# Kernel optimization log

Hardware: AMD Instinct MI355X
Metric: run time of the kernel (lower is better)

## Reference

```python
import jax, jax.numpy as jnp
import numpy as np

N, DIN, D, K, H, N_ITERS = 16384, 256, 1024, 64, 2048, 3
THRESH = 0.3
EPS = 1e-8


def layernorm(x):
    mu = jnp.mean(x, axis=-1, keepdims=True)
    var = jnp.var(x, axis=-1, keepdims=True)
    return (x - mu) * jax.lax.rsqrt(var + 1e-5)


def setup_inputs() -> dict:
    key = jax.random.key(0)
    ks = jax.random.split(key, 20)
    s = 0.02
    return {
        "detections_t": jax.random.normal(ks[0], (N, DIN), jnp.float32),
        "detections_t1": jax.random.normal(ks[1], (N, DIN), jnp.float32),
        "W_enc": s * jax.random.normal(ks[2], (DIN, D), jnp.float32),
        "b_enc": jnp.zeros((D,), jnp.float32),
        "Wq": s * jax.random.normal(ks[3], (D, D), jnp.float32),
        "bq": jnp.zeros((D,), jnp.float32),
        "Wk": s * jax.random.normal(ks[4], (D, D), jnp.float32),
        "bk": jnp.zeros((D,), jnp.float32),
        "Wv": s * jax.random.normal(ks[5], (D, D), jnp.float32),
        "bv": jnp.zeros((D,), jnp.float32),
        "Wi": s * jax.random.normal(ks[6], (3 * D, D), jnp.float32),  # GRU input weights
        "Wh": s * jax.random.normal(ks[7], (3 * D, D), jnp.float32),  # GRU hidden weights
        "bi": jnp.zeros((3 * D,), jnp.float32),
        "bh": jnp.zeros((3 * D,), jnp.float32),
        "W1": s * jax.random.normal(ks[8], (D, H), jnp.float32),
        "b1": jnp.zeros((H,), jnp.float32),
        "W2": s * jax.random.normal(ks[9], (H, D), jnp.float32),
        "b2": jnp.zeros((D,), jnp.float32),
        "slots_mu": s * jax.random.normal(ks[10], (1, D), jnp.float32),
        "init_noise": jax.random.normal(ks[11], (K, D), jnp.float32) * s,
    }


def _gru(u, h, Wi, Wh, bi, bh):
    gi = u @ Wi.T + bi          # [K, 3D]
    gh = h @ Wh.T + bh
    ir, iz, inn = jnp.split(gi, 3, axis=-1)
    hr, hz, hn = jnp.split(gh, 3, axis=-1)
    r = jax.nn.sigmoid(ir + hr)
    z = jax.nn.sigmoid(iz + hz)
    n = jnp.tanh(inn + r * hn)
    return (1.0 - z) * n + z * h


def _process_frame(dets, prev_slots, p):
    x = layernorm(dets @ p["W_enc"] + p["b_enc"])          # [N, D]
    k = x @ p["Wk"] + p["bk"]                               # [N, D]
    v = x @ p["Wv"] + p["bv"]                               # [N, D]
    slots = prev_slots if prev_slots is not None else p["slots_mu"] + p["init_noise"]
    scale = D ** -0.5
    for _ in range(N_ITERS):
        slots_prev = slots
        q = layernorm(slots) @ p["Wq"] + p["bq"]            # [K, D]
        dots = (q @ k.T) * scale                             # [K, N]
        attn = jax.nn.softmax(dots, axis=0)                  # slots compete per detection
        attn = attn / (jnp.sum(attn, axis=-1, keepdims=True) + EPS)
        updates = attn @ v                                   # [K, D]
        slots = _gru(updates, slots_prev, p["Wi"], p["Wh"], p["bi"], p["bh"])
        slots = slots + (jax.nn.relu(layernorm(slots) @ p["W1"] + p["b1"]) @ p["W2"] + p["b2"])
    return slots


def _slot_similarity(a, b):
    an = a / (jnp.linalg.norm(a, axis=-1, keepdims=True) + EPS)
    bn = b / (jnp.linalg.norm(b, axis=-1, keepdims=True) + EPS)
    return an @ bn.T                                         # [K, K]


def _greedy_match(sim):
    max_sims = jnp.max(sim, axis=1)
    max_idxs = jnp.argmax(sim, axis=1)
    order = jnp.argsort(-max_sims)
    def step(carry, idx):
        matches, used = carry
        j = max_idxs[idx]
        ok = jnp.logical_and(~used[j], max_sims[idx] > THRESH)
        matches = matches.at[idx].set(jnp.where(ok, j, matches[idx]))
        used = used.at[j].set(used[j] | ok)
        return (matches, used), None
    init = (jnp.full((K,), -1, jnp.int32), jnp.zeros((K,), jnp.bool_))
    (matches, _), _ = jax.lax.scan(step, init, order)
    return matches


def reference(detections_t, detections_t1, W_enc, b_enc, Wq, bq, Wk, bk, Wv, bv,
              Wi, Wh, bi, bh, W1, b1, W2, b2, slots_mu, init_noise):
    p = dict(W_enc=W_enc, b_enc=b_enc, Wq=Wq, bq=bq, Wk=Wk, bk=bk, Wv=Wv, bv=bv,
             Wi=Wi, Wh=Wh, bi=bi, bh=bh, W1=W1, b1=b1, W2=W2, b2=b2,
             slots_mu=slots_mu, init_noise=init_noise)
    prev_slots = _process_frame(detections_t, None, p)
    curr_slots = _process_frame(detections_t1, prev_slots, p)
    sim = _slot_similarity(prev_slots, curr_slots)
    matches = _greedy_match(sim)
    return matches, sim
```

## Files before the change

kernel.cpp:

```cpp
#include <hip/hip_runtime.h>
#include <hip/hip_bf16.h>
#include <type_traits>

typedef __hip_bfloat16 bf16;
typedef __attribute__((ext_vector_type(8))) short s16x8;
typedef __attribute__((ext_vector_type(4))) float f32x4;

#define N_DET 16384
#define DIN   256
#define DD    1024
#define KSLOT 64
#define HH    2048
#define TD    3072

__device__ __forceinline__ float b2f(bf16 x){ return __bfloat162float(x); }
__device__ __forceinline__ bf16  f2b(float x){ return __float2bfloat16(x); }
__device__ __forceinline__ float bits2f(short u){ return __uint_as_float(((unsigned)(unsigned short)u) << 16); }

__device__ __forceinline__ void gload_lds16(const void* g, void* l) {
  __builtin_amdgcn_global_load_lds(
      (const __attribute__((address_space(1))) unsigned int*)g,
      (__attribute__((address_space(3))) unsigned int*)l, 16, 0, 0);
}

__device__ __forceinline__ void big_compute(bf16* As, bf16* Bs,
    const bf16* __restrict__ Ap, const bf16* __restrict__ Bp, int K, f32x4 acc[4][4])
{
  const int tid = threadIdx.x;
  const int lane = tid & 63, wave = tid >> 6;
  const int wr = wave >> 1, wc = wave & 1;
  const int l15 = lane & 15, h = lane >> 4;
  const int rr = tid >> 3;
  const int qs = ((tid & 7) ^ (rr & 7)) * 8;

#pragma unroll
  for (int m = 0; m < 4; ++m)
#pragma unroll
    for (int n = 0; n < 4; ++n) acc[m][n] = {0.f, 0.f, 0.f, 0.f};

  for (int k0 = 0; k0 < K; k0 += 64) {
    __syncthreads();
#pragma unroll
    for (int g = 0; g < 4; ++g)
      gload_lds16(Ap + (size_t)(g * 32 + rr) * K + k0 + qs,
                  As + ((size_t)g * 256 + wave * 64) * 8);
#pragma unroll
    for (int g = 0; g < 4; ++g)
      gload_lds16(Bp + (size_t)(g * 32 + rr) * K + k0 + qs,
                  Bs + ((size_t)g * 256 + wave * 64) * 8);
    __syncthreads();

#pragma unroll
    for (int ks = 0; ks < 2; ++ks) {
      s16x8 af[4], bfr[4];
#pragma unroll
      for (int m = 0; m < 4; ++m) {
        int row = wr * 64 + m * 16 + l15;
        af[m] = *(const s16x8*)&As[row * 64 + (((ks * 4 + h) ^ (l15 & 7)) * 8)];
      }
#pragma unroll
      for (int n = 0; n < 4; ++n) {
        int row = wc * 64 + n * 16 + l15;
        bfr[n] = *(const s16x8*)&Bs[row * 64 + (((ks * 4 + h) ^ (l15 & 7)) * 8)];
      }
#pragma unroll
      for (int m = 0; m < 4; ++m)
#pragma unroll
        for (int n = 0; n < 4; ++n)
          acc[m][n] = __builtin_amdgcn_mfma_f32_16x16x32_bf16(af[m], bfr[n], acc[m][n], 0, 0, 0);
    }
  }
}

__global__ __launch_bounds__(256) void gemm_mfma_bt(
    const bf16* __restrict__ A, const bf16* __restrict__ Bt,
    const float* __restrict__ bias, bf16* __restrict__ C, int M, int N, int K)
{
  const int nct = N >> 7;
  const int chunk = gridDim.x >> 3;
  const int wg = (blockIdx.x & 7) * chunk + (blockIdx.x >> 3);
  const int bn = (wg % nct) * 128;
  const int bm = (wg / nct) * 128;

  __shared__ bf16 As[128 * 64];
  __shared__ bf16 Bs[128 * 64];
  f32x4 acc[4][4];
  big_compute(As, Bs, A + (size_t)bm * K, Bt + (size_t)bn * K, K, acc);

  const int lane = threadIdx.x & 63, wave = threadIdx.x >> 6;
  const int wr = wave >> 1, wc = wave & 1;
#pragma unroll
  for (int m = 0; m < 4; ++m)
#pragma unroll
    for (int n = 0; n < 4; ++n) {
      int col = bn + wc * 64 + n * 16 + (lane & 15);
      float bv = bias ? bias[col] : 0.f;
#pragma unroll
      for (int j = 0; j < 4; ++j) {
        int row = bm + wr * 64 + m * 16 + (lane >> 4) * 4 + j;
        C[(size_t)row * N + col] = f2b(acc[m][n][j] + bv);
      }
    }
}

__device__ __forceinline__ void skinny_compute(bf16* As, bf16* Bs,
    const bf16* __restrict__ A, const bf16* __restrict__ Bt,
    int K, int Kc, int n0, int kb0, f32x4 acc[4])
{
  const int tid = threadIdx.x;
  const int lane = tid & 63, wave = tid >> 6;
  const int rem = wave * 64 + lane;
  const int r = rem >> 2, q = rem & 3;
  const int l15 = lane & 15, h = lane >> 4;

#pragma unroll
  for (int m = 0; m < 4; ++m) acc[m] = {0.f, 0.f, 0.f, 0.f};

  for (int kb = kb0; kb < kb0 + Kc; kb += 128) {
    __syncthreads();
#pragma unroll
    for (int g = 0; g < 4; ++g)
      gload_lds16(A + (size_t)r * K + kb + g * 32 + q * 8,
                  As + ((size_t)g * 256 + wave * 64) * 8);
#pragma unroll
    for (int g = 0; g < 4; ++g)
      gload_lds16(Bt + (size_t)(n0 + r) * K + kb + g * 32 + q * 8,
                  Bs + ((size_t)g * 256 + wave * 64) * 8);
    __syncthreads();

#pragma unroll
    for (int ks = 0; ks < 4; ++ks) {
      s16x8 bfr = *(const s16x8*)&Bs[(ks * 64 + wave * 16 + l15) * 32 + h * 8];
#pragma unroll
      for (int m = 0; m < 4; ++m) {
        s16x8 af = *(const s16x8*)&As[(ks * 64 + m * 16 + l15) * 32 + h * 8];
        acc[m] = __builtin_amdgcn_mfma_f32_16x16x32_bf16(af, bfr, acc[m], 0, 0, 0);
      }
    }
  }
}

template<int EPI>
__global__ __launch_bounds__(256) void gemm_skinny_e(
    const bf16* __restrict__ A, const bf16* __restrict__ Bt,
    float* __restrict__ pbuf, bf16* __restrict__ outb,
    const float* __restrict__ bias, int N, int K, int Kc)
{
  __shared__ bf16 As[4 * 64 * 32];
  __shared__ bf16 Bs[4 * 64 * 32];
  f32x4 acc[4];
  skinny_compute(As, Bs, A, Bt, K, Kc, blockIdx.x * 64, blockIdx.y * Kc, acc);

  const int lane = threadIdx.x & 63, wave = threadIdx.x >> 6;
  const int l15 = lane & 15, h = lane >> 4;
#pragma unroll
  for (int m = 0; m < 4; ++m)
#pragma unroll
    for (int j = 0; j < 4; ++j) {
      int row = m * 16 + h * 4 + j;
      int col = blockIdx.x * 64 + wave * 16 + l15;
      if (EPI == 0) {
        pbuf[((size_t)(blockIdx.y * 64) + row) * N + col] = acc[m][j];
      } else {
        float v = acc[m][j] + bias[col];
        if (EPI == 2) v = fmaxf(v, 0.f);
        outb[(size_t)row * N + col] = f2b(v);
      }
    }
}

__global__ __launch_bounds__(256) void gemm_skinny_dual(
    const bf16* __restrict__ A0, const bf16* __restrict__ A1,
    const bf16* __restrict__ B0, const bf16* __restrict__ B1,
    float* __restrict__ p0, float* __restrict__ p1, int N, int K, int Kc)
{
  __shared__ bf16 As[4 * 64 * 32];
  __shared__ bf16 Bs[4 * 64 * 32];
  const bf16* A = blockIdx.z ? A1 : A0;
  const bf16* B = blockIdx.z ? B1 : B0;
  float* p = blockIdx.z ? p1 : p0;

  f32x4 acc[4];
  skinny_compute(As, Bs, A, B, K, Kc, blockIdx.x * 64, blockIdx.y * Kc, acc);

  const int lane = threadIdx.x & 63, wave = threadIdx.x >> 6;
  const int l15 = lane & 15, h = lane >> 4;
#pragma unroll
  for (int m = 0; m < 4; ++m)
#pragma unroll
    for (int j = 0; j < 4; ++j) {
      int row = m * 16 + h * 4 + j;
      int col = blockIdx.x * 64 + wave * 16 + l15;
      p[((size_t)(blockIdx.y * 64) + row) * N + col] = acc[m][j];
    }
}

__device__ __forceinline__ void block_ln_store(float v[4], float s, float sq,
    bf16* __restrict__ out, int row,
    const float* __restrict__ wqbk, float* __restrict__ cbuf, float* __restrict__ colsum)
{
  for (int o = 32; o > 0; o >>= 1) { s += __shfl_down(s, o, 64); sq += __shfl_down(sq, o, 64); }
  __shared__ float ls[4], lq[4];
  int w = threadIdx.x >> 6;
  if ((threadIdx.x & 63) == 0) { ls[w] = s; lq[w] = sq; }
  __syncthreads();
  s  = ls[0] + ls[1] + ls[2] + ls[3];
  sq = lq[0] + lq[1] + lq[2] + lq[3];
  float mu = s * (1.f / DD);
  float var = sq * (1.f / DD) - mu * mu;
  float rstd = rsqrtf(var + 1e-5f);
#pragma unroll
  for (int j = 0; j < 4; j++)
    out[(size_t)row * DD + threadIdx.x + j * 256] = f2b((v[j] - mu) * rstd);
  if (wqbk) {
    float dot = 0.f;
#pragma unroll
    for (int j = 0; j < 4; j++) dot += (v[j] - mu) * rstd * wqbk[threadIdx.x + j * 256];
    for (int o = 32; o > 0; o >>= 1) dot += __shfl_down(dot, o, 64);
    __syncthreads();
    if ((threadIdx.x & 63) == 0) ls[w] = dot;
    __syncthreads();
    if (threadIdx.x == 0) { cbuf[row] = ls[0] + ls[1] + ls[2] + ls[3]; colsum[row] = 0.f; }
  }
}

__global__ __launch_bounds__(256) void gru_reduce_ln(const float* __restrict__ pA,
    const float* __restrict__ pB, const float* __restrict__ bvi,
    const float* __restrict__ bh, float* __restrict__ slots, bf16* __restrict__ lnb)
{
  int s = blockIdx.x, t = threadIdx.x;
  float v[4], sum = 0.f, sq = 0.f;
#pragma unroll
  for (int j = 0; j < 4; ++j) {
    int d = t + j * 256;
    const float* a = pA + (size_t)s * TD;
    const float* b = pB + (size_t)s * TD;
    float ir = bvi[d] + a[d], iz = bvi[1024 + d] + a[1024 + d], in_ = bvi[2048 + d] + a[2048 + d];
    float hr = bh[d] + b[d], hz = bh[1024 + d] + b[1024 + d], hnn = bh[2048 + d] + b[2048 + d];
    float r = 1.f / (1.f + expf(-(ir + hr)));
    float z = 1.f / (1.f + expf(-(iz + hz)));
    float nn = tanhf(in_ + r * hnn);
    float h = slots[(size_t)s * DD + d];
    float hv = (1.f - z) * nn + z * h;
    slots[(size_t)s * DD + d] = hv;
    v[j] = hv; sum += hv; sq += hv * hv;
  }
  block_ln_store(v, sum, sq, lnb, s, nullptr, nullptr, nullptr);
}

template<int SK>
__global__ __launch_bounds__(256) void mlp2_reduce_ln(const float* __restrict__ pbuf,
    const float* __restrict__ bias, float* __restrict__ slots,
    bf16* __restrict__ slotspb, bf16* __restrict__ lnb,
    const float* __restrict__ wqbk, float* __restrict__ cbuf, float* __restrict__ colsum)
{
  int s = blockIdx.x, t = threadIdx.x;
  float v[4], sum = 0.f, sq = 0.f;
#pragma unroll
  for (int j = 0; j < 4; ++j) {
    int d = t + j * 256;
    float x = bias[d] + slots[(size_t)s * DD + d];
#pragma unroll
    for (int sk = 0; sk < SK; ++sk) x += pbuf[(size_t)(sk * 64 + s) * DD + d];
    slots[(size_t)s * DD + d] = x;
    slotspb[(size_t)s * DD + d] = f2b(x);
    v[j] = x; sum += x; sq += x * x;
  }
  block_ln_store(v, sum, sq, lnb, s, wqbk, cbuf, colsum);
}

__global__ __launch_bounds__(256) void slots_init_ln(const float* __restrict__ mu,
    const float* __restrict__ noise, float* __restrict__ slots,
    bf16* __restrict__ slotspb, bf16* __restrict__ lnb,
    const float* __restrict__ wqbk, float* __restrict__ cbuf, float* __restrict__ colsum)
{
  int s = blockIdx.x, t = threadIdx.x;
  float v[4], sum = 0.f, sq = 0.f;
#pragma unroll
  for (int j = 0; j < 4; ++j) {
    int d = t + j * 256;
    float x = mu[d] + noise[(size_t)s * DD + d];
    slots[(size_t)s * DD + d] = x;
    slotspb[(size_t)s * DD + d] = f2b(x);
    v[j] = x; sum += x; sq += x * x;
  }
  block_ln_store(v, sum, sq, lnb, s, wqbk, cbuf, colsum);
}

__global__ __launch_bounds__(256) void qk_softmax(const bf16* __restrict__ qkb,
    const bf16* __restrict__ x, const float* __restrict__ cbuf,
    bf16* __restrict__ attn, float* __restrict__ colsum)
{
  __shared__ bf16 Qs[64 * 64];
  __shared__ bf16 Ks[64 * 64];
  __shared__ float cs[64], cl[64];
  const int t = threadIdx.x, lane = t & 63, wave = t >> 6;
  const int n0 = blockIdx.x * 64;
  const int l15 = lane & 15, h = lane >> 4;
  if (t < 64) { cs[t] = 0.f; cl[t] = cbuf[t]; }

  f32x4 acc[4];
#pragma unroll
  for (int m = 0; m < 4; ++m) acc[m] = {0.f, 0.f, 0.f, 0.f};

  for (int k0 = 0; k0 < DD; k0 += 64) {
    __syncthreads();
#pragma unroll
    for (int c = 0; c < 2; ++c) {
      int i = c * 256 + t;
      int r = i >> 3, q8 = i & 7;
      gload_lds16(qkb + (size_t)r * DD + k0 + q8 * 8, Qs + ((size_t)c * 256 + wave * 64) * 8);
    }
#pragma unroll
    for (int c = 0; c < 2; ++c) {
      int i = c * 256 + t;
      int r = i >> 3, q8 = i & 7;
      gload_lds16(x + (size_t)(n0 + r) * DD + k0 + q8 * 8, Ks + ((size_t)c * 256 + wave * 64) * 8);
    }
    __syncthreads();

#pragma unroll
    for (int ks = 0; ks < 2; ++ks) {
      s16x8 bfr = *(const s16x8*)&Ks[(wave * 16 + l15) * 64 + ks * 32 + h * 8];
#pragma unroll
      for (int m = 0; m < 4; ++m) {
        s16x8 af = *(const s16x8*)&Qs[(m * 16 + l15) * 64 + ks * 32 + h * 8];
        acc[m] = __builtin_amdgcn_mfma_f32_16x16x32_bf16(af, bfr, acc[m], 0, 0, 0);
      }
    }
  }

  float e[4][4];
  float cmax = -1e30f;
#pragma unroll
  for (int m = 0; m < 4; ++m)
#pragma unroll
    for (int j = 0; j < 4; ++j) {
      e[m][j] = (acc[m][j] + cl[m * 16 + h * 4 + j]) * 0.03125f;
      cmax = fmaxf(cmax, e[m][j]);
    }
  cmax = fmaxf(cmax, __shfl_xor(cmax, 16, 64));
  cmax = fmaxf(cmax, __shfl_xor(cmax, 32, 64));
  float ssum = 0.f;
#pragma unroll
  for (int m = 0; m < 4; ++m)
#pragma unroll
    for (int j = 0; j < 4; ++j) { e[m][j] = expf(e[m][j] - cmax); ssum += e[m][j]; }
  ssum += __shfl_xor(ssum, 16, 64);
  ssum += __shfl_xor(ssum, 32, 64);
  float inv = 1.f / ssum;
  __syncthreads();

  const int n = n0 + wave * 16 + l15;
#pragma unroll
  for (int m = 0; m < 4; ++m)
#pragma unroll
    for (int j = 0; j < 4; ++j) {
      float a = e[m][j] * inv;
      int s = m * 16 + h * 4 + j;
      attn[(size_t)s * N_DET + n] = f2b(a);
      float v = a;
      v += __shfl_xor(v, 1, 64);
      v += __shfl_xor(v, 2, 64);
      v += __shfl_xor(v, 4, 64);
      v += __shfl_xor(v, 8, 64);
      if (l15 == 0) atomicAdd(&cs[s], v);
    }
  __syncthreads();
  if (t < 64) atomicAdd(&colsum[t], cs[t]);
}

template<int SK>
__global__ __launch_bounds__(256) void updates_reduce2(const float* __restrict__ pbuf,
    const float* __restrict__ colsum, bf16* __restrict__ tb)
{
  int s = blockIdx.y, d = blockIdx.x * 256 + threadIdx.x;
  float v = 0.f;
#pragma unroll
  for (int sk = 0; sk < SK; ++sk) v += pbuf[(size_t)(sk * 64 + s) * DD + d];
  tb[(size_t)s * DD + d] = f2b(v / (colsum[s] + 1e-8f));
}

__global__ __launch_bounds__(256) void transpose_w(const float* __restrict__ W,
                                                   bf16* __restrict__ Wt, int K, int N)
{
  __shared__ float t[32][33];
  int n0 = blockIdx.x * 32, k0 = blockIdx.y * 32;
  int tx = threadIdx.x & 31, ty = threadIdx.x >> 5;
  for (int r = ty; r < 32; r += 8)
    t[r][tx] = W[(size_t)(k0 + r) * N + n0 + tx];
  __syncthreads();
  for (int r = ty; r < 32; r += 8)
    Wt[(size_t)(n0 + r) * K + k0 + tx] = f2b(t[tx][r]);
}

__global__ void f32_to_bf16_v(const float* __restrict__ in, bf16* __restrict__ out, int n)
{
  int i = (blockIdx.x * 256 + threadIdx.x) * 4;
  if (i < n) {
    float4 v = *(const float4*)(in + i);
    bf16 o[4] = {f2b(v.x), f2b(v.y), f2b(v.z), f2b(v.w)};
    *(ushort4*)(out + i) = *(const ushort4*)o;
  }
}

__global__ void convert_all(const float* __restrict__ Wh, const float* __restrict__ Wi,
    const float* __restrict__ Wv, const float* __restrict__ Wq, const float* __restrict__ Wk,
    bf16* __restrict__ oWh, bf16* __restrict__ oWi, bf16* __restrict__ oWv,
    bf16* __restrict__ oWq, bf16* __restrict__ oWk)
{
  int b = blockIdx.x;
  const float* src; bf16* dst; int base;
  if      (b < 3072) { src = Wh; dst = oWh; base = b; }
  else if (b < 6144) { src = Wi; dst = oWi; base = b - 3072; }
  else if (b < 7168) { src = Wv; dst = oWv; base = b - 6144; }
  else if (b < 8192) { src = Wq; dst = oWq; base = b - 7168; }
  else               { src = Wk; dst = oWk; base = b - 8192; }
  int i = (base * 256 + threadIdx.x) * 4;
  float4 v = *(const float4*)(src + i);
  bf16 o[4] = {f2b(v.x), f2b(v.y), f2b(v.z), f2b(v.w)};
  *(ushort4*)(dst + i) = *(const ushort4*)o;
}

__global__ void matvec3(const float* __restrict__ Wi, const float* __restrict__ Wq,
    const float* __restrict__ Wk, const float* __restrict__ bv, const float* __restrict__ bk,
    const float* __restrict__ bq, const float* __restrict__ bi,
    float* __restrict__ bvi, float* __restrict__ wqbk, float* __restrict__ bqk)
{
  int i = blockIdx.x * 256 + threadIdx.x;
  const float* w; const float* vec; float s; float* out; int idx;
  if (i < 3072)      { idx = i;        w = Wi + (size_t)idx * DD; vec = bv; s = bi[idx]; out = bvi; }
  else if (i < 4096) { idx = i - 3072; w = Wq + (size_t)idx * DD; vec = bk; s = 0.f;     out = wqbk; }
  else               { idx = i - 4096; w = Wk + (size_t)idx * DD; vec = bq; s = 0.f;     out = bqk; }
  for (int k = 0; k < DD; k += 4) {
    float4 wv = *(const float4*)(w + k);
    float4 bb = *(const float4*)(vec + k);
    s += wv.x * bb.x + wv.y * bb.y + wv.z * bb.z + wv.w * bb.w;
  }
  out[idx] = s;
}

__global__ __launch_bounds__(256) void transpose_x(const bf16* __restrict__ in, bf16* __restrict__ out)
{
  __shared__ bf16 t[64][72];
  int n0 = blockIdx.x * 64, d0 = blockIdx.y * 64;
  int r = threadIdx.x >> 2, c = (threadIdx.x & 3) * 16;
  s16x8 v0 = *(const s16x8*)&in[(size_t)(n0 + r) * DD + d0 + c];
  s16x8 v1 = *(const s16x8*)&in[(size_t)(n0 + r) * DD + d0 + c + 8];
  const bf16* p0 = (const bf16*)&v0;
  const bf16* p1 = (const bf16*)&v1;
#pragma unroll
  for (int j = 0; j < 8; ++j) { t[c + j][r] = p0[j]; t[c + 8 + j][r] = p1[j]; }
  __syncthreads();
  bf16 o[16];
#pragma unroll
  for (int j = 0; j < 16; ++j) o[j] = t[r][c + j];
  *(s16x8*)&out[(size_t)(d0 + r) * N_DET + n0 + c]     = *(const s16x8*)&o[0];
  *(s16x8*)&out[(size_t)(d0 + r) * N_DET + n0 + c + 8] = *(const s16x8*)&o[8];
}

__global__ __launch_bounds__(256) void ln_rows2(const bf16* __restrict__ in, bf16* __restrict__ out)
{
  int r = blockIdx.x * 2 + (threadIdx.x >> 7);
  int t7 = threadIdx.x & 127;
  s16x8 vv = *(const s16x8*)(in + (size_t)r * DD + t7 * 8);
  float f[8], s = 0.f, sq = 0.f;
#pragma unroll
  for (int j = 0; j < 8; ++j) { f[j] = bits2f(vv[j]); s += f[j]; sq += f[j] * f[j]; }
  for (int o = 32; o > 0; o >>= 1) { s += __shfl_down(s, o, 64); sq += __shfl_down(sq, o, 64); }
  __shared__ float ls[4], lq[4];
  int w = threadIdx.x >> 6;
  if ((threadIdx.x & 63) == 0) { ls[w] = s; lq[w] = sq; }
  __syncthreads();
  int rg = threadIdx.x >> 7;
  s  = ls[rg * 2] + ls[rg * 2 + 1];
  sq = lq[rg * 2] + lq[rg * 2 + 1];
  float mu = s * (1.f / DD);
  float var = sq * (1.f / DD) - mu * mu;
  float rstd = rsqrtf(var + 1e-5f);
  bf16 o[8];
#pragma unroll
  for (int j = 0; j < 8; ++j) o[j] = f2b((f[j] - mu) * rstd);
  *(s16x8*)(out + (size_t)r * DD + t7 * 8) = *(const s16x8*)o;
}

__global__ __launch_bounds__(256) void rownorm2(const float* __restrict__ a,
    const float* __restrict__ b, float* __restrict__ an, float* __restrict__ bn)
{
  int rb = blockIdx.x;
  const float* p = (rb < 64 ? a : b) + (size_t)(rb & 63) * DD;
  float* o = (rb < 64 ? an : bn) + (size_t)(rb & 63) * DD;
  float v[4], sq = 0.f;
#pragma unroll
  for (int j = 0; j < 4; j++) { v[j] = p[threadIdx.x + j*256]; sq += v[j]*v[j]; }
  for (int os = 32; os > 0; os >>= 1) sq += __shfl_down(sq, os, 64);
  __shared__ float lq[4];
  int w = threadIdx.x >> 6;
  if ((threadIdx.x & 63) == 0) lq[w] = sq;
  __syncthreads();
  sq = lq[0] + lq[1] + lq[2] + lq[3];
  float sc = 1.f / (sqrtf(sq) + 1e-8f);
#pragma unroll
  for (int j = 0; j < 4; j++) o[threadIdx.x + j*256] = v[j] * sc;
}

__global__ __launch_bounds__(256) void sim_kernel(const float* __restrict__ an,
    const float* __restrict__ bn, float* __restrict__ simout)
{
  __shared__ float ar[1024];
  int i = blockIdx.x;
  for (int l = threadIdx.x; l < 1024; l += 256) ar[l] = an[(size_t)i * DD + l];
  __syncthreads();
  int j = threadIdx.x >> 2, g = threadIdx.x & 3;
  float sum = 0.f;
  for (int d = g; d < 1024; d += 4) sum += ar[d] * bn[(size_t)j * DD + d];
  sum += __shfl_xor(sum, 1, 64);
  sum += __shfl_xor(sum, 2, 64);
  if (g == 0) simout[i * 64 + j] = sum;
}

__global__ void match_kernel(const float* __restrict__ sim, float* __restrict__ outm)
{
  __shared__ float m[64];
  __shared__ int idx[64];
  __shared__ int order[64];
  __shared__ int used[64];
  int i = threadIdx.x;
  float best = -1e30f; int bj = 0;
  for (int j = 0; j < 64; j++) {
    float v = sim[i * 64 + j];
    if (v > best) { best = v; bj = j; }
  }
  m[i] = best; idx[i] = bj; used[i] = 0;
  __syncthreads();
  int cnt = 0;
  for (int j = 0; j < 64; j++) {
    float mj = m[j];
    if (mj > best || (mj == best && j < i)) cnt++;
  }
  order[cnt] = i;
  __syncthreads();
  if (i == 0) {
    for (int r = 0; r < 64; r++) {
      int ii = order[r];
      int j = idx[ii];
      bool ok = (!used[j]) && (m[ii] > 0.3f);
      outm[ii] = ok ? (float)j : -1.0f;
      if (ok) used[j] = 1;
    }
  }
}

static constexpr size_t OFF_XPRE = 0;
static constexpr size_t OFF_ATT  = 0;
static constexpr size_t OFF_PA   = (size_t)4  << 20;
static constexpr size_t OFF_P0   = (size_t)8  << 20;
static constexpr size_t OFF_P1   = (size_t)10 << 20;
static constexpr size_t OFF_WET  = (size_t)32 << 20;
static constexpr size_t OFF_WQKT = OFF_WET + ((size_t)512 << 10);
static constexpr size_t OFF_W1T  = OFF_WQKT + ((size_t)2 << 20);
static constexpr size_t OFF_W2T  = OFF_W1T + ((size_t)4 << 20);
static constexpr size_t OFF_WHB  = OFF_W2T + ((size_t)4 << 20);
static constexpr size_t OFF_WVIT = OFF_WHB + ((size_t)6 << 20);
static constexpr size_t OFF_X    = (size_t)60 << 20;
static constexpr size_t OFF_WIB  = OFF_X;
static constexpr size_t OFF_WVB  = OFF_X + ((size_t)6 << 20);
static constexpr size_t OFF_WQB  = OFF_X + ((size_t)8 << 20);
static constexpr size_t OFF_WKB  = OFF_X + ((size_t)10 << 20);
static constexpr size_t OFF_DBF  = OFF_X;
static constexpr size_t OFF_XT   = OFF_X + ((size_t)32 << 20);
static constexpr size_t OFF_SM   = OFF_XT + ((size_t)32 << 20);
static constexpr size_t OFF_SL   = OFF_SM;
static constexpr size_t OFF_SLPB = OFF_SL  + 262144;
static constexpr size_t OFF_LNB  = OFF_SLPB + 131072;
static constexpr size_t OFF_QKB  = OFF_LNB + 131072;
static constexpr size_t OFF_TB   = OFF_QKB + 131072;
static constexpr size_t OFF_HIDB = OFF_TB  + 131072;
static constexpr size_t OFF_PRV  = OFF_HIDB + 262144;
static constexpr size_t OFF_AN   = OFF_PRV + 262144;
static constexpr size_t OFF_BN   = OFF_AN  + 262144;
static constexpr size_t OFF_CS   = OFF_BN  + 262144;
static constexpr size_t OFF_BVI  = OFF_CS  + 4096;
static constexpr size_t OFF_WQBK = OFF_BVI + 16384;
static constexpr size_t OFF_BQK  = OFF_WQBK + 4096;

extern "C" void kernel_launch(void* const* d_in, const int* in_sizes, int n_in,
                              void* d_out, int out_size, void* d_ws, size_t ws_size,
                              hipStream_t stream)
{
  (void)in_sizes; (void)n_in; (void)out_size; (void)ws_size;
  const float* dets_t   = (const float*)d_in[0];
  const float* dets_t1  = (const float*)d_in[1];
  const float* W_enc    = (const float*)d_in[2];
  const float* b_enc    = (const float*)d_in[3];
  const float* Wq       = (const float*)d_in[4];
  const float* bq       = (const float*)d_in[5];
  const float* Wk       = (const float*)d_in[6];
  const float* bk       = (const float*)d_in[7];
  const float* Wv       = (const float*)d_in[8];
  const float* bv       = (const float*)d_in[9];
  const float* Wi       = (const float*)d_in[10];
  const float* Wh       = (const float*)d_in[11];
  const float* bi       = (const float*)d_in[12];
  const float* bh       = (const float*)d_in[13];
  const float* W1       = (const float*)d_in[14];
  const float* b1       = (const float*)d_in[15];
  const float* W2       = (const float*)d_in[16];
  const float* b2       = (const float*)d_in[17];
  const float* slots_mu = (const float*)d_in[18];
  const float* init_noise = (const float*)d_in[19];

  char* ws = (char*)d_ws;
  bf16*  x_pre  = (bf16*)(ws + OFF_XPRE);
  bf16*  attn   = (bf16*)(ws + OFF_ATT);
  float* pA     = (float*)(ws + OFF_PA);
  float* p0     = (float*)(ws + OFF_P0);
  float* p1     = (float*)(ws + OFF_P1);
  bf16*  Wenc_t = (bf16*)(ws + OFF_WET);
  bf16*  Wqk_t  = (bf16*)(ws + OFF_WQKT);
  bf16*  W1_t   = (bf16*)(ws + OFF_W1T);
  bf16*  W2_t   = (bf16*)(ws + OFF_W2T);
  bf16*  Wh_b   = (bf16*)(ws + OFF_WHB);
  bf16*  Wvit   = (bf16*)(ws + OFF_WVIT);
  bf16*  Wi_b   = (bf16*)(ws + OFF_WIB);
  bf16*  Wv_bf  = (bf16*)(ws + OFF_WVB);
  bf16*  Wq_bf  = (bf16*)(ws + OFF_WQB);
  bf16*  Wk_bf  = (bf16*)(ws + OFF_WKB);
  bf16*  dets_bf= (bf16*)(ws + OFF_DBF);
  bf16*  x      = (bf16*)(ws + OFF_X);
  bf16*  xT     = (bf16*)(ws + OFF_XT);
  float* slots  = (float*)(ws + OFF_SL);
  bf16*  slotspb= (bf16*)(ws + OFF_SLPB);
  bf16*  lnb    = (bf16*)(ws + OFF_LNB);
  bf16*  qkb    = (bf16*)(ws + OFF_QKB);
  bf16*  tb     = (bf16*)(ws + OFF_TB);
  bf16*  hidb   = (bf16*)(ws + OFF_HIDB);
  float* prevs  = (float*)(ws + OFF_PRV);
  float* an     = (float*)(ws + OFF_AN);
  float* bn     = (float*)(ws + OFF_BN);
  float* colsum = (float*)(ws + OFF_CS);
  float* cbuf   = colsum + 64;
  float* bvi    = (float*)(ws + OFF_BVI);
  float* wqbk   = (float*)(ws + OFF_WQBK);
  float* bqk    = (float*)(ws + OFF_BQK);

  transpose_w<<<dim3(32,  8), 256, 0, stream>>>(W_enc, Wenc_t, DIN, DD);
  transpose_w<<<dim3(64, 32), 256, 0, stream>>>(W1,    W1_t,   DD,  HH);
  transpose_w<<<dim3(32, 64), 256, 0, stream>>>(W2,    W2_t,   HH,  DD);
  convert_all<<<9216, 256, 0, stream>>>(Wh, Wi, Wv, Wq, Wk, Wh_b, Wi_b, Wv_bf, Wq_bf, Wk_bf);
  matvec3<<<20, 256, 0, stream>>>(Wi, Wq, Wk, bv, bk, bq, bi, bvi, wqbk, bqk);
  gemm_mfma_bt<<<192, 256, 0, stream>>>(Wi_b, Wv_bf, nullptr, Wvit, TD, DD, DD);
  gemm_mfma_bt<<<64, 256, 0, stream>>>(Wk_bf, Wq_bf, nullptr, Wqk_t, DD, DD, DD);

  auto frame = [&](const float* dets, bool first) {
    f32_to_bf16_v<<<(N_DET*DIN)/1024, 256, 0, stream>>>(dets, dets_bf, N_DET*DIN);
    gemm_mfma_bt<<<1024, 256, 0, stream>>>(dets_bf, Wenc_t, b_enc, x_pre, N_DET, DD, DIN);
    ln_rows2<<<N_DET/2, 256, 0, stream>>>(x_pre, x);
    transpose_x<<<dim3(256, 16), 256, 0, stream>>>(x, xT);
    if (first) slots_init_ln<<<64, 256, 0, stream>>>(slots_mu, init_noise, slots, slotspb, lnb, wqbk, cbuf, colsum);
    for (int it = 0; it < 3; ++it) {
      gemm_skinny_e<1><<<dim3(16, 1), 256, 0, stream>>>(lnb, Wqk_t, nullptr, qkb, bqk, DD, DD, DD);
      qk_softmax<<<256, 256, 0, stream>>>(qkb, x, cbuf, attn, colsum);
      gemm_skinny_e<0><<<dim3(16, 16), 256, 0, stream>>>(attn, xT, pA, nullptr, nullptr, DD, N_DET, 1024);
      updates_reduce2<16><<<dim3(4, 64), 256, 0, stream>>>(pA, colsum, tb);
      gemm_skinny_dual<<<dim3(48, 1, 2), 256, 0, stream>>>(tb, slotspb, Wvit, Wh_b, p0, p1, TD, DD, DD);
      gru_reduce_ln<<<64, 256, 0, stream>>>(p0, p1, bvi, bh, slots, lnb);
      gemm_skinny_e<2><<<dim3(32, 1), 256, 0, stream>>>(lnb, W1_t, nullptr, hidb, b1, HH, DD, DD);
      gemm_skinny_e<0><<<dim3(16, 2), 256, 0, stream>>>(hidb, W2_t, pA, nullptr, nullptr, DD, HH, 1024);
      mlp2_reduce_ln<2><<<64, 256, 0, stream>>>(pA, b2, slots, slotspb, lnb, wqbk, cbuf, colsum);
    }
  };

  frame(dets_t, true);
  hipMemcpyAsync(prevs, slots, 262144, hipMemcpyDeviceToDevice, stream);
  frame(dets_t1, false);

  rownorm2<<<128, 256, 0, stream>>>(prevs, slots, an, bn);
  float* outf = (float*)d_out;
  sim_kernel<<<KSLOT, 256, 0, stream>>>(an, bn, outf + 64);
  match_kernel<<<1, 64, 0, stream>>>(outf + 64, outf);
}
```

Before: 752.8 us.

## Fuse setup kernels, parallelize matvec per wave, and fuse layernorm with transpose

Merges the three weight transposes into one launch and the two setup GEMMs into one launch. The bias matvec now gives one wavefront per row with coalesced loads, where before each thread walked a whole row serially. Per frame, layernorm and the transpose of x are fused into one kernel that stages 32 rows in LDS and writes both x and xT. This removes a round trip of x through global memory and several launches, but the column reads from the LDS tile in the transpose phase may hit bank conflicts and the large LDS tile limits occupancy.

```diff
diff --git a/kernel.cpp b/kernel.cpp
--- a/kernel.cpp
+++ b/kernel.cpp
@@ -72,18 +72,13 @@
   }
 }
 
-__global__ __launch_bounds__(256) void gemm_mfma_bt(
+__device__ __forceinline__ void big_gemm_body(int wg, int nct,
     const bf16* __restrict__ A, const bf16* __restrict__ Bt,
-    const float* __restrict__ bias, bf16* __restrict__ C, int M, int N, int K)
-{
-  const int nct = N >> 7;
-  const int chunk = gridDim.x >> 3;
-  const int wg = (blockIdx.x & 7) * chunk + (blockIdx.x >> 3);
+    const float* __restrict__ bias, bf16* __restrict__ C, int N, int K,
+    bf16* As, bf16* Bs)
+{
   const int bn = (wg % nct) * 128;
   const int bm = (wg / nct) * 128;
-
-  __shared__ bf16 As[128 * 64];
-  __shared__ bf16 Bs[128 * 64];
   f32x4 acc[4][4];
   big_compute(As, Bs, A + (size_t)bm * K, Bt + (size_t)bn * K, K, acc);
 
@@ -101,6 +96,35 @@
         C[(size_t)row * N + col] = f2b(acc[m][n][j] + bv);
       }
     }
+}
+
+__global__ __launch_bounds__(256) void gemm_mfma_bt(
+    const bf16* __restrict__ A, const bf16* __restrict__ Bt,
+    const float* __restrict__ bias, bf16* __restrict__ C, int M, int N, int K)
+{
+  const int nct = N >> 7;
+  const int chunk = gridDim.x >> 3;
+  const int wg = (blockIdx.x & 7) * chunk + (blockIdx.x >> 3);
+  __shared__ bf16 As[128 * 64];
+  __shared__ bf16 Bs[128 * 64];
+  big_gemm_body(wg, nct, A, Bt, bias, C, N, K, As, Bs);
+}
+
+__global__ __launch_bounds__(256) void gemm_setup_pair(
+    const bf16* __restrict__ Wi_b, const bf16* __restrict__ Wv_bf, bf16* __restrict__ Wvit,
+    const bf16* __restrict__ Wk_bf, const bf16* __restrict__ Wq_bf, bf16* __restrict__ Wqk_t)
+{
+  __shared__ bf16 As[128 * 64];
+  __shared__ bf16 Bs[128 * 64];
+  if (blockIdx.x < 192) {
+    int bid = blockIdx.x;
+    int wg = (bid & 7) * 24 + (bid >> 3);
+    big_gemm_body(wg, 8, Wi_b, Wv_bf, nullptr, Wvit, DD, DD, As, Bs);
+  } else {
+    int bid = blockIdx.x - 192;
+    int wg = (bid & 7) * 8 + (bid >> 3);
+    big_gemm_body(wg, 8, Wk_bf, Wq_bf, nullptr, Wqk_t, DD, DD, As, Bs);
+  }
 }
 
 __device__ __forceinline__ void skinny_compute(bf16* As, bf16* Bs,
@@ -381,11 +405,17 @@
   tb[(size_t)s * DD + d] = f2b(v / (colsum[s] + 1e-8f));
 }
 
-__global__ __launch_bounds__(256) void transpose_w(const float* __restrict__ W,
-                                                   bf16* __restrict__ Wt, int K, int N)
+__global__ __launch_bounds__(256) void transpose_all(const float* __restrict__ W_enc,
+    const float* __restrict__ W1, const float* __restrict__ W2,
+    bf16* __restrict__ Wenc_t, bf16* __restrict__ W1_t, bf16* __restrict__ W2_t)
 {
   __shared__ float t[32][33];
-  int n0 = blockIdx.x * 32, k0 = blockIdx.y * 32;
+  int b = blockIdx.x;
+  const float* W; bf16* Wt; int K, N, bx, by;
+  if (b < 256)       { W = W_enc; Wt = Wenc_t; K = DIN;  N = DD; bx = b & 31;  by = b >> 5; }
+  else if (b < 2304) { int r = b - 256;  W = W1; Wt = W1_t; K = DD;  N = HH; bx = r & 63; by = r >> 6; }
+  else               { int r = b - 2304; W = W2; Wt = W2_t; K = HH;  N = DD; bx = r & 31; by = r >> 5; }
+  int n0 = bx * 32, k0 = by * 32;
   int tx = threadIdx.x & 31, ty = threadIdx.x >> 5;
   for (int r = ty; r < 32; r += 8)
     t[r][tx] = W[(size_t)(k0 + r) * N + n0 + tx];
@@ -422,66 +452,90 @@
   *(ushort4*)(dst + i) = *(const ushort4*)o;
 }
 
-__global__ void matvec3(const float* __restrict__ Wi, const float* __restrict__ Wq,
-    const float* __restrict__ Wk, const float* __restrict__ bv, const float* __restrict__ bk,
-    const float* __restrict__ bq, const float* __restrict__ bi,
+__global__ __launch_bounds__(256) void matvec3_wave(const float* __restrict__ Wi,
+    const float* __restrict__ Wq, const float* __restrict__ Wk,
+    const float* __restrict__ bv, const float* __restrict__ bk, const float* __restrict__ bq,
+    const float* __restrict__ bi,
     float* __restrict__ bvi, float* __restrict__ wqbk, float* __restrict__ bqk)
 {
-  int i = blockIdx.x * 256 + threadIdx.x;
-  const float* w; const float* vec; float s; float* out; int idx;
-  if (i < 3072)      { idx = i;        w = Wi + (size_t)idx * DD; vec = bv; s = bi[idx]; out = bvi; }
-  else if (i < 4096) { idx = i - 3072; w = Wq + (size_t)idx * DD; vec = bk; s = 0.f;     out = wqbk; }
-  else               { idx = i - 4096; w = Wk + (size_t)idx * DD; vec = bq; s = 0.f;     out = bqk; }
-  for (int k = 0; k < DD; k += 4) {
-    float4 wv = *(const float4*)(w + k);
-    float4 bb = *(const float4*)(vec + k);
+  int row = blockIdx.x * 4 + (threadIdx.x >> 6);
+  int lane = threadIdx.x & 63;
+  const float* w; const float* vec; float s0; float* out; int idx;
+  if (row < 3072)      { idx = row;        w = Wi + (size_t)idx * DD; vec = bv; s0 = bi[idx]; out = bvi; }
+  else if (row < 4096) { idx = row - 3072; w = Wq + (size_t)idx * DD; vec = bk; s0 = 0.f;     out = wqbk; }
+  else                 { idx = row - 4096; w = Wk + (size_t)idx * DD; vec = bq; s0 = 0.f;     out = bqk; }
+  float s = 0.f;
+#pragma unroll
+  for (int c = 0; c < 4; ++c) {
+    float4 wv = *(const float4*)(w + c * 256 + lane * 4);
+    float4 bb = *(const float4*)(vec + c * 256 + lane * 4);
     s += wv.x * bb.x + wv.y * bb.y + wv.z * bb.z + wv.w * bb.w;
   }
-  out[idx] = s;
-}
-
-__global__ __launch_bounds__(256) void transpose_x(const bf16* __restrict__ in, bf16* __restrict__ out)
-{
-  __shared__ bf16 t[64][72];
-  int n0 = blockIdx.x * 64, d0 = blockIdx.y * 64;
-  int r = threadIdx.x >> 2, c = (threadIdx.x & 3) * 16;
-  s16x8 v0 = *(const s16x8*)&in[(size_t)(n0 + r) * DD + d0 + c];
-  s16x8 v1 = *(const s16x8*)&in[(size_t)(n0 + r) * DD + d0 + c + 8];
-  const bf16* p0 = (const bf16*)&v0;
-  const bf16* p1 = (const bf16*)&v1;
-#pragma unroll
-  for (int j = 0; j < 8; ++j) { t[c + j][r] = p0[j]; t[c + 8 + j][r] = p1[j]; }
-  __syncthreads();
-  bf16 o[16];
-#pragma unroll
-  for (int j = 0; j < 16; ++j) o[j] = t[r][c + j];
-  *(s16x8*)&out[(size_t)(d0 + r) * N_DET + n0 + c]     = *(const s16x8*)&o[0];
-  *(s16x8*)&out[(size_t)(d0 + r) * N_DET + n0 + c + 8] = *(const s16x8*)&o[8];
-}
-
-__global__ __launch_bounds__(256) void ln_rows2(const bf16* __restrict__ in, bf16* __restrict__ out)
-{
-  int r = blockIdx.x * 2 + (threadIdx.x >> 7);
-  int t7 = threadIdx.x & 127;
-  s16x8 vv = *(const s16x8*)(in + (size_t)r * DD + t7 * 8);
-  float f[8], s = 0.f, sq = 0.f;
-#pragma unroll
-  for (int j = 0; j < 8; ++j) { f[j] = bits2f(vv[j]); s += f[j]; sq += f[j] * f[j]; }
-  for (int o = 32; o > 0; o >>= 1) { s += __shfl_down(s, o, 64); sq += __shfl_down(sq, o, 64); }
-  __shared__ float ls[4], lq[4];
-  int w = threadIdx.x >> 6;
-  if ((threadIdx.x & 63) == 0) { ls[w] = s; lq[w] = sq; }
-  __syncthreads();
-  int rg = threadIdx.x >> 7;
-  s  = ls[rg * 2] + ls[rg * 2 + 1];
-  sq = lq[rg * 2] + lq[rg * 2 + 1];
-  float mu = s * (1.f / DD);
-  float var = sq * (1.f / DD) - mu * mu;
-  float rstd = rsqrtf(var + 1e-5f);
-  bf16 o[8];
-#pragma unroll
-  for (int j = 0; j < 8; ++j) o[j] = f2b((f[j] - mu) * rstd);
-  *(s16x8*)(out + (size_t)r * DD + t7 * 8) = *(const s16x8*)o;
+  for (int o = 32; o > 0; o >>= 1) s += __shfl_down(s, o, 64);
+  if (lane == 0) out[idx] = s0 + s;
+}
+
+__global__ __launch_bounds__(256) void ln_transpose(const bf16* __restrict__ x_pre,
+    bf16* __restrict__ x, bf16* __restrict__ xT)
+{
+  __shared__ bf16 tile[32][1032];
+  __shared__ float mus[32], rs[32];
+  const int t = threadIdx.x;
+  const int n0 = blockIdx.x * 32;
+
+#pragma unroll
+  for (int i = 0; i < 16; ++i) {
+    int flat = i * 256 + t;
+    int row = flat >> 7, c8 = flat & 127;
+    *(s16x8*)&tile[row][c8 * 8] = *(const s16x8*)&x_pre[(size_t)(n0 + row) * DD + c8 * 8];
+  }
+  __syncthreads();
+
+  {
+    int row = t >> 3, part = t & 7;
+    float s = 0.f, sq = 0.f;
+#pragma unroll
+    for (int kk = 0; kk < 16; ++kk) {
+      s16x8 v = *(const s16x8*)&tile[row][part * 128 + kk * 8];
+#pragma unroll
+      for (int j = 0; j < 8; ++j) { float f = bits2f(v[j]); s += f; sq += f * f; }
+    }
+    s  += __shfl_xor(s, 1, 64);  sq += __shfl_xor(sq, 1, 64);
+    s  += __shfl_xor(s, 2, 64);  sq += __shfl_xor(sq, 2, 64);
+    s  += __shfl_xor(s, 4, 64);  sq += __shfl_xor(sq, 4, 64);
+    if (part == 0) {
+      float mu = s * (1.f / DD);
+      float var = sq * (1.f / DD) - mu * mu;
+      mus[row] = mu;
+      rs[row] = rsqrtf(var + 1e-5f);
+    }
+  }
+  __syncthreads();
+
+#pragma unroll
+  for (int i = 0; i < 16; ++i) {
+    int flat = i * 256 + t;
+    int row = flat >> 7, c8 = flat & 127;
+    float mu = mus[row], r = rs[row];
+    s16x8 v = *(const s16x8*)&tile[row][c8 * 8];
+    bf16 o[8];
+#pragma unroll
+    for (int j = 0; j < 8; ++j) o[j] = f2b((bits2f(v[j]) - mu) * r);
+    *(s16x8*)&x[(size_t)(n0 + row) * DD + c8 * 8] = *(const s16x8*)o;
+  }
+
+#pragma unroll
+  for (int i = 0; i < 16; ++i) {
+    int flat = i * 256 + t;
+    int d = flat >> 2, ch = flat & 3;
+    bf16 o[8];
+#pragma unroll
+    for (int k = 0; k < 8; ++k) {
+      int nl = ch * 8 + k;
+      o[k] = f2b((b2f(tile[nl][d]) - mus[nl]) * rs[nl]);
+    }
+    *(s16x8*)&xT[(size_t)d * N_DET + n0 + ch * 8] = *(const s16x8*)o;
+  }
 }
 
 __global__ __launch_bounds__(256) void rownorm2(const float* __restrict__ a,
@@ -644,19 +698,15 @@
   float* wqbk   = (float*)(ws + OFF_WQBK);
   float* bqk    = (float*)(ws + OFF_BQK);
 
-  transpose_w<<<dim3(32,  8), 256, 0, stream>>>(W_enc, Wenc_t, DIN, DD);
-  transpose_w<<<dim3(64, 32), 256, 0, stream>>>(W1,    W1_t,   DD,  HH);
-  transpose_w<<<dim3(32, 64), 256, 0, stream>>>(W2,    W2_t,   HH,  DD);
+  transpose_all<<<4352, 256, 0, stream>>>(W_enc, W1, W2, Wenc_t, W1_t, W2_t);
   convert_all<<<9216, 256, 0, stream>>>(Wh, Wi, Wv, Wq, Wk, Wh_b, Wi_b, Wv_bf, Wq_bf, Wk_bf);
-  matvec3<<<20, 256, 0, stream>>>(Wi, Wq, Wk, bv, bk, bq, bi, bvi, wqbk, bqk);
-  gemm_mfma_bt<<<192, 256, 0, stream>>>(Wi_b, Wv_bf, nullptr, Wvit, TD, DD, DD);
-  gemm_mfma_bt<<<64, 256, 0, stream>>>(Wk_bf, Wq_bf, nullptr, Wqk_t, DD, DD, DD);
+  matvec3_wave<<<1280, 256, 0, stream>>>(Wi, Wq, Wk, bv, bk, bq, bi, bvi, wqbk, bqk);
+  gemm_setup_pair<<<256, 256, 0, stream>>>(Wi_b, Wv_bf, Wvit, Wk_bf, Wq_bf, Wqk_t);
 
   auto frame = [&](const float* dets, bool first) {
     f32_to_bf16_v<<<(N_DET*DIN)/1024, 256, 0, stream>>>(dets, dets_bf, N_DET*DIN);
     gemm_mfma_bt<<<1024, 256, 0, stream>>>(dets_bf, Wenc_t, b_enc, x_pre, N_DET, DD, DIN);
-    ln_rows2<<<N_DET/2, 256, 0, stream>>>(x_pre, x);
-    transpose_x<<<dim3(256, 16), 256, 0, stream>>>(x, xT);
+    ln_transpose<<<512, 256, 0, stream>>>(x_pre, x, xT);
     if (first) slots_init_ln<<<64, 256, 0, stream>>>(slots_mu, init_noise, slots, slotspb, lnb, wqbk, cbuf, colsum);
     for (int it = 0; it < 3; ++it) {
       gemm_skinny_e<1><<<dim3(16, 1), 256, 0, stream>>>(lnb, Wqk_t, nullptr, qkb, bqk, DD, DD, DD);
```

Result: faster. 667.0 us (-11.4%).
